# Kernel optimization log

Measured on AMD Instinct MI355X. Metric: run time of the kernel, lower is better.

The kernel has to match this reference:

```python
import jax, jax.numpy as jnp
import numpy as np

B, L, C, N = 8, 1024, 1024, 5000


def setup_inputs() -> dict:
    key = jax.random.key(0)
    k1, k2, k3 = jax.random.split(key, 3)
    z = jax.random.normal(k1, (B, L, C), dtype=jnp.float32)
    codebook = jax.random.normal(k2, (N, C), dtype=jnp.float32)
    mask = jax.random.bernoulli(k3, 0.9, (B, L))  # bool [B, L]
    return {"z": z, "mask": mask, "codebook": codebook}


def reference(z, mask, codebook):
    # pairwise squared L2 distance via the GEMM identity:
    # ||z - c||^2 = ||z||^2 + ||c||^2 - 2 z.c   (same math as broadcast-subtract-square-sum)
    z2 = jnp.sum(z * z, axis=-1, keepdims=True)        # [B, L, 1]
    c2 = jnp.sum(codebook * codebook, axis=-1)         # [N]
    cross = jnp.einsum('blc,nc->bln', z, codebook)     # [B, L, N]
    distance = z2 + c2 - 2.0 * cross                   # [B, L, N]
    indices = jnp.argmin(distance, axis=-1)            # [B, L] int
    quantized = codebook[indices]                      # gather -> [B, L, C]
    quantized = jnp.where(mask[..., None], quantized, 0.0)  # quantized[~mask] = 0
    commit_loss = jnp.float32(0.0)
    return quantized, indices, commit_loss
```

## Files before the change

kernel.cpp:

```cpp
#include <hip/hip_runtime.h>
#include <stdint.h>


#define M_TOTAL  8192
#define K_DIM    1024
#define N_REAL   5000
#define N_PAD    5120
#define NB_CNT   40
#define SLOTS    6
#define MARGIN   8.0f

typedef __attribute__((ext_vector_type(8))) short bf16x8;
typedef __attribute__((ext_vector_type(4))) float f32x4;
typedef unsigned long long u64;

__device__ __forceinline__ ushort f2bf(float x) {
  union { float f; uint32_t u; } v; v.f = x;
  uint32_t r = v.u + 0x7FFFu + ((v.u >> 16) & 1u);
  return (ushort)(r >> 16);
}

__device__ __forceinline__ void async16(void* lds, const void* g) {
  __builtin_amdgcn_global_load_lds(
      (const __attribute__((address_space(1))) void*)g,
      (__attribute__((address_space(3))) void*)lds, 16, 0, 0);
}

__device__ __forceinline__ uint32_t fenc(float f) {
  union { float f; uint32_t u; } v; v.f = f;
  return v.u ^ ((v.u >> 31) ? 0xFFFFFFFFu : 0x80000000u);
}
__device__ __forceinline__ float fdec(uint32_t e) {
  uint32_t u = e ^ ((e & 0x80000000u) ? 0x80000000u : 0xFFFFFFFFu);
  union { uint32_t u; float f; } v; v.u = u; return v.f;
}


__global__ __launch_bounds__(256) void convert_z(const float4* __restrict__ z4,
                                                 ushort* __restrict__ zb, int n4) {
  int i = blockIdx.x * blockDim.x + threadIdx.x;
  int stride = gridDim.x * blockDim.x;
  for (; i < n4; i += stride) {
    float4 v = z4[i];
    ushort4 u;
    u.x = f2bf(v.x); u.y = f2bf(v.y); u.z = f2bf(v.z); u.w = f2bf(v.w);
    *(ushort4*)&zb[(size_t)i * 4] = u;
  }
}

__global__ __launch_bounds__(256) void prep_cb(const float* __restrict__ cb,
                                               ushort* __restrict__ cbb,
                                               float* __restrict__ c2) {
  __shared__ float sred[4];
  const int row = blockIdx.x;
  const int tid = threadIdx.x;
  if (row >= N_REAL) {
    ushort4 zz; zz.x = zz.y = zz.z = zz.w = 0;
    *(ushort4*)&cbb[(size_t)row * K_DIM + tid * 4] = zz;
    if (tid == 0) c2[row] = 0.f;
    return;
  }
  float4 v = ((const float4*)(cb + (size_t)row * K_DIM))[tid];
  ushort4 u;
  u.x = f2bf(v.x); u.y = f2bf(v.y); u.z = f2bf(v.z); u.w = f2bf(v.w);
  *(ushort4*)&cbb[(size_t)row * K_DIM + tid * 4] = u;
  float s = v.x * v.x + v.y * v.y + v.z * v.z + v.w * v.w;
  #pragma unroll
  for (int off = 32; off; off >>= 1) s += __shfl_down(s, off);
  int wv = tid >> 6, ln = tid & 63;
  if (ln == 0) sred[wv] = s;
  __syncthreads();
  if (tid == 0) c2[row] = sred[0] + sred[1] + sred[2] + sred[3];
}


__global__ __launch_bounds__(256) void gemm_score(const ushort* __restrict__ A,
                                                  const ushort* __restrict__ Bm,
                                                  const float* __restrict__ c2,
                                                  u64* __restrict__ cand) {
  __shared__ __align__(16) char smem[32768];
  ushort* sA = (ushort*)smem;
  ushort* sB = (ushort*)(smem + 16384);
  u64 (*scand)[SLOTS] = (u64 (*)[SLOTS])smem;
  int* scnt = (int*)(smem + 6144);

  const int tid  = threadIdx.x;
  const int wave = tid >> 6, lane = tid & 63;
  const int wm = wave >> 1, wn = wave & 1;
  const int tM = blockIdx.y * 128;
  const int tN = blockIdx.x * 128;
  const int nb = blockIdx.x;

  f32x4 acc[4][4];
  #pragma unroll
  for (int i = 0; i < 4; ++i)
    #pragma unroll
    for (int j = 0; j < 4; ++j)
      acc[i][j] = (f32x4)0.f;

  char* sAb = (char*)sA;
  char* sBb = (char*)sB;
  const int o = tid * 16;

  for (int k0 = 0; k0 < K_DIM; k0 += 64) {
    __syncthreads();
    #pragma unroll
    for (int it = 0; it < 4; ++it) {
      int ob = o + it * 4096;
      int r  = ob >> 7;
      int cbyte = ob & 127;
      const char* ga = (const char*)A + ((size_t)(tM + r) * K_DIM + k0) * 2 + cbyte;
      async16(sAb + ob, ga);
      const char* gb = (const char*)Bm + ((size_t)(tN + r) * K_DIM + k0) * 2 + cbyte;
      async16(sBb + ob, gb);
    }
    __syncthreads();
    #pragma unroll
    for (int kk = 0; kk < 2; ++kk) {
      bf16x8 af[4], bfr[4];
      const int kcol = kk * 32 + (lane >> 4) * 8;
      #pragma unroll
      for (int f = 0; f < 4; ++f) {
        int ra = wm * 64 + f * 16 + (lane & 15);
        af[f]  = *(const bf16x8*)&sA[ra * 64 + kcol];
        int rb = wn * 64 + f * 16 + (lane & 15);
        bfr[f] = *(const bf16x8*)&sB[rb * 64 + kcol];
      }
      #pragma unroll
      for (int i = 0; i < 4; ++i)
        #pragma unroll
        for (int j = 0; j < 4; ++j)
          acc[i][j] = __builtin_amdgcn_mfma_f32_16x16x32_bf16(af[i], bfr[j], acc[i][j], 0, 0, 0);
    }
  }

  __syncthreads();
  if (tid < 128) {
    scnt[tid] = 0;
    #pragma unroll
    for (int s = 0; s < SLOTS; ++s) scand[tid][s] = ~0ull;
  }
  __syncthreads();

  const int cl = lane & 15, rg = lane >> 4;
  int   ncol[4];
  float c2v[4];
  #pragma unroll
  for (int j = 0; j < 4; ++j) {
    ncol[j] = tN + wn * 64 + j * 16 + cl;
    c2v[j]  = (ncol[j] < N_REAL) ? c2[ncol[j]] : 0.f;
  }

  #pragma unroll
  for (int i = 0; i < 4; ++i) {
    #pragma unroll
    for (int r = 0; r < 4; ++r) {
      float bv = 3.4e38f; int bc = 0x7fffffff;
      #pragma unroll
      for (int j = 0; j < 4; ++j) {
        float sc = (ncol[j] < N_REAL) ? (c2v[j] - 2.0f * acc[i][j][r]) : 3.4e38f;
        if (sc < bv || (sc == bv && ncol[j] < bc)) { bv = sc; bc = ncol[j]; }
      }
      #pragma unroll
      for (int off = 1; off < 16; off <<= 1) {
        float ov = __shfl_xor(bv, off);
        int   oc = __shfl_xor(bc, off);
        if (ov < bv || (ov == bv && oc < bc)) { bv = ov; bc = oc; }
      }
      if (cl == 0) {
        const int lr = wm * 64 + i * 16 + rg * 4 + r;
        u64 pk = ((u64)fenc(bv) << 32) | (uint32_t)bc;
        atomicMin(&scand[lr][0], pk);
      }
    }
  }
  __syncthreads();

  #pragma unroll
  for (int i = 0; i < 4; ++i) {
    #pragma unroll
    for (int r = 0; r < 4; ++r) {
      const int lr = wm * 64 + i * 16 + rg * 4 + r;
      const u64 mn = scand[lr][0];
      const float thr  = fdec((uint32_t)(mn >> 32)) + MARGIN;
      const int mincol = (int)(mn & 0xFFFFFFFFu);
      #pragma unroll
      for (int j = 0; j < 4; ++j) {
        if (ncol[j] < N_REAL) {
          float sc = c2v[j] - 2.0f * acc[i][j][r];
          if (sc <= thr && ncol[j] != mincol) {
            int p = atomicAdd(&scnt[lr], 1);
            if (p < SLOTS - 1)
              scand[lr][1 + p] = ((u64)fenc(sc) << 32) | (uint32_t)ncol[j];
          }
        }
      }
    }
  }
  __syncthreads();

  if (tid < 128) {
    const size_t base = ((size_t)(tM + tid) * NB_CNT + nb) * SLOTS;
    #pragma unroll
    for (int s = 0; s < SLOTS; ++s) cand[base + s] = scand[tid][s];
  }
}


__global__ __launch_bounds__(256) void finalize(const u64* __restrict__ cand,
                                                const float* __restrict__ z,
                                                const float* __restrict__ cb,
                                                const int* __restrict__ mask,
                                                float* __restrict__ out_q,
                                                float* __restrict__ out_i,
                                                float* __restrict__ out_loss) {
  __shared__ u64 swm[4];
  __shared__ float sthr;
  __shared__ int scols[64];
  __shared__ int scnt2;
  __shared__ double sdv[4];
  __shared__ double sbestd;
  __shared__ int    sbesti;

  const int tid = threadIdx.x;
  const int m   = blockIdx.x;
  const int wv = tid >> 6, ln = tid & 63;
  const u64* row = cand + (size_t)m * (NB_CNT * SLOTS);

  const u64 e = (tid < NB_CNT * SLOTS) ? row[tid] : ~0ull;

  u64 g = (tid < NB_CNT * SLOTS && (tid % SLOTS) == 0) ? e : ~0ull;
  #pragma unroll
  for (int off = 32; off; off >>= 1) {
    u64 o = __shfl_down(g, off);
    if (o < g) g = o;
  }
  if (ln == 0) swm[wv] = g;
  __syncthreads();
  if (tid == 0) {
    u64 gg = swm[0];
    for (int w = 1; w < 4; ++w) if (swm[w] < gg) gg = swm[w];
    sthr = fdec((uint32_t)(gg >> 32)) + MARGIN;
    scnt2 = 0;
  }
  __syncthreads();

  if (tid < NB_CNT * SLOTS) {
    float sc = fdec((uint32_t)(e >> 32));
    if (sc <= sthr) {
      int p = atomicAdd(&scnt2, 1);
      if (p < 64) scols[p] = (int)(e & 0xFFFFFFFFu);
    }
  }
  __syncthreads();
  int nc = scnt2 < 64 ? scnt2 : 64;

  if (tid == 0) { sbestd = 1e300; sbesti = 0x7fffffff; }
  __syncthreads();
  const float4 zv = ((const float4*)(z + (size_t)m * K_DIM))[tid];
  for (int c = 0; c < nc; ++c) {
    const int n = scols[c];
    float4 cv = ((const float4*)(cb + (size_t)n * K_DIM))[tid];
    double lsum = (double)cv.x * ((double)cv.x - 2.0 * (double)zv.x)
                + (double)cv.y * ((double)cv.y - 2.0 * (double)zv.y)
                + (double)cv.z * ((double)cv.z - 2.0 * (double)zv.z)
                + (double)cv.w * ((double)cv.w - 2.0 * (double)zv.w);
    #pragma unroll
    for (int off = 32; off; off >>= 1) lsum += __shfl_down(lsum, off);
    if (ln == 0) sdv[wv] = lsum;
    __syncthreads();
    if (tid == 0) {
      double s = sdv[0] + sdv[1] + sdv[2] + sdv[3];
      if (s < sbestd || (s == sbestd && n < sbesti)) { sbestd = s; sbesti = n; }
    }
    __syncthreads();
  }

  const int bidx = sbesti;
  if (tid == 0) out_i[m] = (float)bidx;
  const int mk = mask[m];
  float4 qz; qz.x = qz.y = qz.z = qz.w = 0.f;
  float4 src = ((const float4*)(cb + (size_t)bidx * K_DIM))[tid];
  ((float4*)(out_q + (size_t)m * K_DIM))[tid] = mk ? src : qz;
  if (m == 0 && tid == 0) *out_loss = 0.0f;
}


extern "C" void kernel_launch(void* const* d_in, const int* in_sizes, int n_in,
                              void* d_out, int out_size, void* d_ws, size_t ws_size,
                              hipStream_t stream) {
  const float* z    = (const float*)d_in[0];
  const int*   mask = (const int*)d_in[1];
  const float* cb   = (const float*)d_in[2];

  float* out      = (float*)d_out;
  float* out_q    = out;
  float* out_i    = out + (size_t)M_TOTAL * K_DIM;
  float* out_loss = out_i + M_TOTAL;

  char* ws = (char*)d_ws;
  ushort* zb   = (ushort*)(ws);
  ushort* cbb  = (ushort*)(ws + 16777216);
  float*  c2   = (float*)(ws + 27262976);
  u64*    cand = (u64*)(ws + 27283456);

  convert_z<<<2048, 256, 0, stream>>>((const float4*)z, zb, (M_TOTAL * K_DIM) / 4);
  prep_cb<<<N_PAD, 256, 0, stream>>>(cb, cbb, c2);

  dim3 g(N_PAD / 128, M_TOTAL / 128);
  gemm_score<<<g, 256, 0, stream>>>(zb, cbb, c2, cand);
  finalize<<<M_TOTAL, 256, 0, stream>>>(cand, z, cb, mask, out_q, out_i, out_loss);
}
```

Measured before the change: 312.2 us.

## Enlarge GEMM tile to 256x256 with 512 threads and double-buffered LDS

Moves the distance GEMM from 128x128 tiles with 4 waves to 256x256 tiles with 8 waves, each wave computing a 128x64 sub-tile. The K loop now uses two LDS buffers so async global-to-LDS loads for the next K slice overlap MFMA work on the current one. The aim is higher arithmetic intensity and hidden load latency. The cost is 128KB of LDS and more accumulators per thread, which limits occupancy to one block per CU and may spill registers. The grid becomes 20x32 blocks, and the candidate buffer count NB_CNT is halved to match.

```diff
diff --git a/kernel.cpp b/kernel.cpp
--- a/kernel.cpp
+++ b/kernel.cpp
@@ -6,7 +6,7 @@
 #define K_DIM    1024
 #define N_REAL   5000
 #define N_PAD    5120
-#define NB_CNT   40
+#define NB_CNT   20
 #define SLOTS    6
 #define MARGIN   8.0f
 
@@ -74,68 +74,77 @@
 }
 
 
-__global__ __launch_bounds__(256) void gemm_score(const ushort* __restrict__ A,
+__global__ __launch_bounds__(512) void gemm_score(const ushort* __restrict__ A,
                                                   const ushort* __restrict__ Bm,
                                                   const float* __restrict__ c2,
                                                   u64* __restrict__ cand) {
-  __shared__ __align__(16) char smem[32768];
-  ushort* sA = (ushort*)smem;
-  ushort* sB = (ushort*)(smem + 16384);
-  u64 (*scand)[SLOTS] = (u64 (*)[SLOTS])smem;
-  int* scnt = (int*)(smem + 6144);
+  __shared__ __align__(16) char smem[131072];
 
   const int tid  = threadIdx.x;
   const int wave = tid >> 6, lane = tid & 63;
-  const int wm = wave >> 1, wn = wave & 1;
-  const int tM = blockIdx.y * 128;
-  const int tN = blockIdx.x * 128;
+  const int wm = wave >> 2, wn = wave & 3;
+  const int tM = blockIdx.y * 256;
+  const int tN = blockIdx.x * 256;
   const int nb = blockIdx.x;
 
-  f32x4 acc[4][4];
-  #pragma unroll
-  for (int i = 0; i < 4; ++i)
+  f32x4 acc[8][4];
+  #pragma unroll
+  for (int i = 0; i < 8; ++i)
     #pragma unroll
     for (int j = 0; j < 4; ++j)
       acc[i][j] = (f32x4)0.f;
 
-  char* sAb = (char*)sA;
-  char* sBb = (char*)sB;
   const int o = tid * 16;
 
-  for (int k0 = 0; k0 < K_DIM; k0 += 64) {
-    __syncthreads();
+  auto stage = [&](int b, int k0) {
+    char* dstA = smem + b * 65536;
+    char* dstB = dstA + 32768;
     #pragma unroll
     for (int it = 0; it < 4; ++it) {
-      int ob = o + it * 4096;
+      int ob = o + it * 8192;
       int r  = ob >> 7;
       int cbyte = ob & 127;
-      const char* ga = (const char*)A + ((size_t)(tM + r) * K_DIM + k0) * 2 + cbyte;
-      async16(sAb + ob, ga);
-      const char* gb = (const char*)Bm + ((size_t)(tN + r) * K_DIM + k0) * 2 + cbyte;
-      async16(sBb + ob, gb);
-    }
-    __syncthreads();
+      async16(dstA + ob, (const char*)A  + ((size_t)(tM + r) * K_DIM + k0) * 2 + cbyte);
+      async16(dstB + ob, (const char*)Bm + ((size_t)(tN + r) * K_DIM + k0) * 2 + cbyte);
+    }
+  };
+
+  auto compute = [&](int b) {
+    const ushort* sA = (const ushort*)(smem + b * 65536);
+    const ushort* sB = (const ushort*)(smem + b * 65536 + 32768);
     #pragma unroll
     for (int kk = 0; kk < 2; ++kk) {
-      bf16x8 af[4], bfr[4];
       const int kcol = kk * 32 + (lane >> 4) * 8;
-      #pragma unroll
-      for (int f = 0; f < 4; ++f) {
-        int ra = wm * 64 + f * 16 + (lane & 15);
-        af[f]  = *(const bf16x8*)&sA[ra * 64 + kcol];
-        int rb = wn * 64 + f * 16 + (lane & 15);
-        bfr[f] = *(const bf16x8*)&sB[rb * 64 + kcol];
-      }
-      #pragma unroll
-      for (int i = 0; i < 4; ++i)
+      bf16x8 af[8], bfr[4];
+      #pragma unroll
+      for (int f = 0; f < 8; ++f)
+        af[f] = *(const bf16x8*)&sA[(wm * 128 + f * 16 + (lane & 15)) * 64 + kcol];
+      #pragma unroll
+      for (int f = 0; f < 4; ++f)
+        bfr[f] = *(const bf16x8*)&sB[(wn * 64 + f * 16 + (lane & 15)) * 64 + kcol];
+      #pragma unroll
+      for (int i = 0; i < 8; ++i)
         #pragma unroll
         for (int j = 0; j < 4; ++j)
           acc[i][j] = __builtin_amdgcn_mfma_f32_16x16x32_bf16(af[i], bfr[j], acc[i][j], 0, 0, 0);
     }
-  }
-
-  __syncthreads();
-  if (tid < 128) {
+  };
+
+  stage(0, 0);
+  __syncthreads();
+  int cur = 0;
+  for (int t = 0; t < (K_DIM / 64) - 1; ++t) {
+    stage(cur ^ 1, (t + 1) * 64);
+    compute(cur);
+    __syncthreads();
+    cur ^= 1;
+  }
+  compute(cur);
+
+  __syncthreads();
+  u64 (*scand)[SLOTS] = (u64 (*)[SLOTS])smem;
+  int* scnt = (int*)(smem + 12288);
+  if (tid < 256) {
     scnt[tid] = 0;
     #pragma unroll
     for (int s = 0; s < SLOTS; ++s) scand[tid][s] = ~0ull;
@@ -152,7 +161,7 @@
   }
 
   #pragma unroll
-  for (int i = 0; i < 4; ++i) {
+  for (int i = 0; i < 8; ++i) {
     #pragma unroll
     for (int r = 0; r < 4; ++r) {
       float bv = 3.4e38f; int bc = 0x7fffffff;
@@ -168,7 +177,7 @@
         if (ov < bv || (ov == bv && oc < bc)) { bv = ov; bc = oc; }
       }
       if (cl == 0) {
-        const int lr = wm * 64 + i * 16 + rg * 4 + r;
+        const int lr = wm * 128 + i * 16 + rg * 4 + r;
         u64 pk = ((u64)fenc(bv) << 32) | (uint32_t)bc;
         atomicMin(&scand[lr][0], pk);
       }
@@ -177,10 +186,10 @@
   __syncthreads();
 
   #pragma unroll
-  for (int i = 0; i < 4; ++i) {
+  for (int i = 0; i < 8; ++i) {
     #pragma unroll
     for (int r = 0; r < 4; ++r) {
-      const int lr = wm * 64 + i * 16 + rg * 4 + r;
+      const int lr = wm * 128 + i * 16 + rg * 4 + r;
       const u64 mn = scand[lr][0];
       const float thr  = fdec((uint32_t)(mn >> 32)) + MARGIN;
       const int mincol = (int)(mn & 0xFFFFFFFFu);
@@ -199,7 +208,7 @@
   }
   __syncthreads();
 
-  if (tid < 128) {
+  if (tid < 256) {
     const size_t base = ((size_t)(tM + tid) * NB_CNT + nb) * SLOTS;
     #pragma unroll
     for (int s = 0; s < SLOTS; ++s) cand[base + s] = scand[tid][s];
@@ -307,7 +316,7 @@
   convert_z<<<2048, 256, 0, stream>>>((const float4*)z, zb, (M_TOTAL * K_DIM) / 4);
   prep_cb<<<N_PAD, 256, 0, stream>>>(cb, cbb, c2);
 
-  dim3 g(N_PAD / 128, M_TOTAL / 128);
-  gemm_score<<<g, 256, 0, stream>>>(zb, cbb, c2, cand);
+  dim3 g(N_PAD / 256, M_TOTAL / 256);
+  gemm_score<<<g, 512, 0, stream>>>(zb, cbb, c2, cand);
   finalize<<<M_TOTAL, 256, 0, stream>>>(cand, z, cb, mask, out_q, out_i, out_loss);
 }
```

Result: faster. 297.4 us (-4.7%).
